# Performance work log

Hardware: AMD Instinct MI355X
Metric: run time of the kernel (lower is better)

Reference implementation:

```python
import jax, jax.numpy as jnp
import numpy as np

EPS = 1e-6
TEMP_GEO = 0.07
W_LOCAL = 0.5
W_SHARP = 0.5


def _l2norm(x):
    return x / jnp.clip(jnp.linalg.norm(x, axis=-1, keepdims=True), 1e-12)


def setup_inputs() -> dict:
    key = jax.random.key(0)
    ks = jax.random.split(key, 6)
    B, L, S, C = 8, 1024, 1024, 128
    N, P = 8, 256
    q_geo = _l2norm(jax.random.normal(ks[0], (B, L, C), jnp.float32))
    geo_pos = _l2norm(jax.random.normal(ks[1], (B, S, C), jnp.float32))
    label = jax.random.randint(ks[2], (B, L, S), 0, 2, jnp.int32)
    q_cl = jax.random.normal(ks[3], (N, P, C), jnp.float32)
    cl_pos = jax.random.normal(ks[4], (N, P, C), jnp.float32)
    idx = jax.random.randint(ks[5], (N,), 0, P, jnp.int32)
    return {"q_geo": q_geo, "q_cl": q_cl, "geo_pos": geo_pos,
            "cl_pos": cl_pos, "label": label, "idx": idx}


def _masked_mean(v, m):
    # per-sample mean over the [L,S] plane of entries where m is True
    m = m.astype(v.dtype)
    return jnp.sum(v * m, axis=(1, 2)) / jnp.maximum(jnp.sum(m, axis=(1, 2)), 1.0)


def _loftr_loss(conf, label):
    # standard LoFTR coarse CE loss (LoFTRLoss source absent from repo snippet)
    conf = jnp.clip(conf, EPS, 1.0 - EPS)
    pos = label == 1
    neg = label == 0
    pos_loss = _masked_mean(-jnp.log(conf), pos)          # [B]
    neg_loss = _masked_mean(-jnp.log(1.0 - conf), neg)    # [B]
    loss = pos_loss + neg_loss
    return jnp.mean(loss), jnp.mean(pos_loss), jnp.mean(neg_loss)


def _geometric_loss(q, k, label):
    sim = jnp.einsum('blc,bsc->bls', q, k) / TEMP_GEO        # [B,L,S]
    conf = jax.nn.softmax(sim, axis=1) * jax.nn.softmax(sim, axis=2)
    return _loftr_loss(conf, label)


def _sharpness_loss(q, k, label):
    sim = (1.0 + jnp.einsum('blc,bsc->bls', q, k)) / 2.0     # [B,L,S]
    # column stats (over L, dim=0 per sample) -> sharpness1 [B,S]
    s1 = (jnp.max(sim, axis=1) - jnp.mean(sim, axis=1)) / jnp.std(sim, axis=1, ddof=1)
    sharp1 = jax.nn.softmax(s1, axis=-1)
    # row stats (over S, dim=1 per sample) -> sharpness2 [B,L]
    s2 = (jnp.max(sim, axis=2) - jnp.mean(sim, axis=2)) / jnp.std(sim, axis=2, ddof=1)
    sharp2 = jax.nn.softmax(s2, axis=-1)
    simc = jnp.clip(sim, EPS, 1.0 - EPS)
    nll = -jnp.log(simc)
    pos = (label == 1).astype(simc.dtype)
    neg = (label == 0)
    loss1 = jnp.sum(nll * sharp1[:, None, :] * pos, axis=(1, 2))   # [B]
    loss2 = jnp.sum(nll * sharp2[:, :, None] * pos, axis=(1, 2))   # [B]
    loss3 = _masked_mean(-jnp.log(1.0 - simc), neg)                # [B]
    losses = (loss1 + loss2) / 2.0 + loss3
    return sharp1, jnp.mean(losses)


def _contrast_loss(q, all_k):
    # intended math of GeCoContrast: full cosine matrix, diag positives, tail negatives
    N = q.shape[0]
    sim = (1.0 + _l2norm(q) @ _l2norm(all_k).T) / 2.0   # [N, M]
    sim = jnp.clip(sim, EPS, 1.0 - EPS)
    l_pos = jnp.diagonal(sim[:, :N])                    # [N]
    l_neg = sim[:, N:]                                  # [N, M-N]
    return (jnp.mean(-jnp.log(l_pos)) + jnp.mean(-jnp.log(1.0 - l_neg))) / 2.0


def _forward(q_geo, q_cl, geo_pos, cl_pos, label, idx):
    loss_geo, geo_pos_loss, geo_neg_loss = _geometric_loss(q_geo, geo_pos, label)
    sharpness, loss_sharp = _sharpness_loss(q_geo, geo_pos, label)
    loss_geo = ((1.0 - W_SHARP) * loss_geo + W_SHARP * loss_sharp) * W_LOCAL

    N, P, C = q_cl.shape
    ar = jnp.arange(N)
    q_sel = q_cl[ar, idx]                               # [N,C]
    sel = cl_pos[ar, idx]                               # [N,C] positives moved to slot 0
    first = cl_pos[:, 0, :]
    swapped = cl_pos.at[ar, idx].set(first).at[:, 0, :].set(sel)
    cl_pos_save = sel
    all_k = jnp.concatenate([swapped[:, 0, :],
                             swapped[:, 1:, :].reshape(N * (P - 1), C)], axis=0)
    loss_cl = _contrast_loss(q_sel, all_k) * (1.0 - W_LOCAL)

    total = loss_geo + loss_cl
    return (sharpness, cl_pos_save, total, geo_pos_loss, geo_neg_loss, loss_sharp, loss_cl)


def reference(q_geo, q_cl, geo_pos, cl_pos, label, idx):
    return _forward(q_geo, q_cl, geo_pos, cl_pos, label, idx)
```

## Files before the change

kernel.cpp:

```cpp
#include <hip/hip_runtime.h>
#include <math.h>

#define BB 8
#define LL 1024
#define SS 1024
#define CC 128
#define NN 8
#define PP 256

static constexpr float EPS       = 1e-6f;
static constexpr float ONE_M_EPS = 1.0f - 1e-6f;
static constexpr float INV_T     = 1.0f / 0.07f;
static constexpr float NLL_MAX   = 13.815511f;
static constexpr float NLL_MIN   = 1.0000005e-6f;

static constexpr size_t DOTSZ      = (size_t)BB * LL * SS;
static constexpr size_t OFF_LSER   = DOTSZ;
static constexpr size_t OFF_LSEC   = DOTSZ + 16384;
static constexpr size_t OFF_SHARP2 = DOTSZ + 32768;
static constexpr size_t OFF_RP     = DOTSZ + 40960;
static constexpr size_t OFF_CP     = OFF_RP + 1048576;
static constexpr size_t OFF_ACC    = OFF_CP + 524288;
static constexpr size_t OFF_ACCCL  = OFF_ACC + 48;
static constexpr size_t OFF_QN     = OFF_ACC + 64;

static constexpr int OUT_CLSAVE = 8192;
static constexpr int OUT_SCAL   = 9216;

typedef __bf16 bf16x8 __attribute__((ext_vector_type(8)));
typedef float  floatx4 __attribute__((ext_vector_type(4)));

__device__ __forceinline__ void split_f4(float4 x,
                                         unsigned& hp0, unsigned& hp1,
                                         unsigned& lp0, unsigned& lp1) {
    unsigned u0 = __builtin_bit_cast(unsigned, x.x);
    unsigned u1 = __builtin_bit_cast(unsigned, x.y);
    unsigned u2 = __builtin_bit_cast(unsigned, x.z);
    unsigned u3 = __builtin_bit_cast(unsigned, x.w);
    unsigned r0 = u0 + 0x7FFFu + ((u0 >> 16) & 1u);
    unsigned r1 = u1 + 0x7FFFu + ((u1 >> 16) & 1u);
    unsigned r2 = u2 + 0x7FFFu + ((u2 >> 16) & 1u);
    unsigned r3 = u3 + 0x7FFFu + ((u3 >> 16) & 1u);
    float s0 = x.x - __builtin_bit_cast(float, r0 & 0xFFFF0000u);
    float s1 = x.y - __builtin_bit_cast(float, r1 & 0xFFFF0000u);
    float s2 = x.z - __builtin_bit_cast(float, r2 & 0xFFFF0000u);
    float s3 = x.w - __builtin_bit_cast(float, r3 & 0xFFFF0000u);
    hp0 = __builtin_amdgcn_perm(r1, r0, 0x07060302u);
    hp1 = __builtin_amdgcn_perm(r3, r2, 0x07060302u);
    lp0 = __builtin_amdgcn_perm(__builtin_bit_cast(unsigned, s1),
                                __builtin_bit_cast(unsigned, s0), 0x07060302u);
    lp1 = __builtin_amdgcn_perm(__builtin_bit_cast(unsigned, s3),
                                __builtin_bit_cast(unsigned, s2), 0x07060302u);
}

__global__ __launch_bounds__(512) void gemm_dot(const float* __restrict__ A,
                                                const float* __restrict__ Bm,
                                                const float* __restrict__ q_cl,
                                                const float* __restrict__ cl_pos,
                                                const int* __restrict__ idx,
                                                float* __restrict__ out,
                                                float* __restrict__ dot,
                                                float* __restrict__ ws) {
    __shared__ __align__(16) char lds[65536];

    int tid  = threadIdx.x;
    int lane = tid & 63;
    int w    = tid >> 6;

    if (blockIdx.x == 512) {
        if (tid < 52) ws[OFF_ACC + tid] = 0.0f;
        int n = w;
        if (n < NN) {
            int in = idx[n];
            const float* q = q_cl + ((size_t)(n * PP + in)) * CC;
            float2 qv = *(const float2*)(q + 2 * lane);
            float ss = qv.x * qv.x + qv.y * qv.y;
            for (int o = 32; o; o >>= 1) ss += __shfl_xor(ss, o);
            float inv = 1.0f / fmaxf(sqrtf(ss), 1e-12f);
            *(float2*)(ws + OFF_QN + n * 128 + 2 * lane) = make_float2(qv.x * inv, qv.y * inv);
            const float* cp = cl_pos + ((size_t)(n * PP + in)) * CC;
            float2 cv = *(const float2*)(cp + 2 * lane);
            *(float2*)(out + OUT_CLSAVE + n * 128 + 2 * lane) = cv;
        }
        return;
    }

    int t  = blockIdx.x;
    int b  = t >> 6;
    int rm = t & 63;
    int bl = rm >> 3, bs = rm & 7;
    int R0 = bl * 128, C0 = bs * 128;

    const float* Ab = A  + ((size_t)(b * 1024 + R0)) * CC;
    const float* Bb = Bm + ((size_t)(b * 1024 + C0)) * CC;

    const float* srcu[2];
    int hib[2], lob[2];
#pragma unroll
    for (int u = 0; u < 2; u++) {
        int g   = u * 512 + tid;
        int mat = g >> 9;
        int r   = (g >> 2) & 127;
        int c8  = g & 3;
        srcu[u] = (mat ? Bb : Ab) + (size_t)r * CC + c8 * 8;
        int base = mat * 16384 + r * 128;
        int sw   = r & 7;
        hib[u] = base + ((c8 ^ sw) * 16);
        lob[u] = base + (((c8 + 4) ^ sw) * 16);
    }

    int fl   = lane & 15;
    int quad = lane >> 4;
    int wr   = w >> 2, wc = w & 3;
    int Rw   = wr * 64, Cw = wc * 32;

    floatx4 acc[4][2];
#pragma unroll
    for (int i = 0; i < 4; i++)
#pragma unroll
        for (int j = 0; j < 2; j++) acc[i][j] = (floatx4){0.f, 0.f, 0.f, 0.f};

    float4 e0[2], e1[2], o0[2], o1[2];
#pragma unroll
    for (int u = 0; u < 2; u++) {
        e0[u] = *(const float4*)(srcu[u]);
        e1[u] = *(const float4*)(srcu[u] + 4);
        o0[u] = *(const float4*)(srcu[u] + 32);
        o1[u] = *(const float4*)(srcu[u] + 36);
    }
#pragma unroll
    for (int u = 0; u < 2; u++) {
        unsigned h0, h1, h2, h3, l0, l1, l2, l3;
        split_f4(e0[u], h0, h1, l0, l1); split_f4(e1[u], h2, h3, l2, l3);
        *(uint4*)(&lds[hib[u]]) = make_uint4(h0, h1, h2, h3);
        *(uint4*)(&lds[lob[u]]) = make_uint4(l0, l1, l2, l3);
        split_f4(o0[u], h0, h1, l0, l1); split_f4(o1[u], h2, h3, l2, l3);
        *(uint4*)(&lds[32768 + hib[u]]) = make_uint4(h0, h1, h2, h3);
        *(uint4*)(&lds[32768 + lob[u]]) = make_uint4(l0, l1, l2, l3);
    }
    __syncthreads();

#pragma unroll
    for (int half = 0; half < 2; half++) {
        if (half == 0) {
#pragma unroll
            for (int u = 0; u < 2; u++) {
                e0[u] = *(const float4*)(srcu[u] + 64);
                e1[u] = *(const float4*)(srcu[u] + 68);
                o0[u] = *(const float4*)(srcu[u] + 96);
                o1[u] = *(const float4*)(srcu[u] + 100);
            }
        }
#pragma unroll
        for (int kk = 0; kk < 2; kk++) {
            const char* la = lds + kk * 32768;
            const char* lb = la + 16384;
            bf16x8 ah[4], al[4];
#pragma unroll
            for (int mt = 0; mt < 4; mt++) {
                int row = Rw + mt * 16 + fl;
                int sw  = row & 7;
                ah[mt] = *(const bf16x8*)(la + row * 128 + ((quad ^ sw) * 16));
                al[mt] = *(const bf16x8*)(la + row * 128 + (((quad + 4) ^ sw) * 16));
            }
#pragma unroll
            for (int nt = 0; nt < 2; nt++) {
                int row = Cw + nt * 16 + fl;
                int sw  = row & 7;
                bf16x8 bh  = *(const bf16x8*)(lb + row * 128 + ((quad ^ sw) * 16));
                bf16x8 blo = *(const bf16x8*)(lb + row * 128 + (((quad + 4) ^ sw) * 16));
#pragma unroll
                for (int mt = 0; mt < 4; mt++) {
                    acc[mt][nt] = __builtin_amdgcn_mfma_f32_16x16x32_bf16(ah[mt], bh,  acc[mt][nt], 0, 0, 0);
                    acc[mt][nt] = __builtin_amdgcn_mfma_f32_16x16x32_bf16(ah[mt], blo, acc[mt][nt], 0, 0, 0);
                    acc[mt][nt] = __builtin_amdgcn_mfma_f32_16x16x32_bf16(al[mt], bh,  acc[mt][nt], 0, 0, 0);
                }
            }
        }
        __syncthreads();
        if (half == 0) {
#pragma unroll
            for (int u = 0; u < 2; u++) {
                unsigned h0, h1, h2, h3, l0, l1, l2, l3;
                split_f4(e0[u], h0, h1, l0, l1); split_f4(e1[u], h2, h3, l2, l3);
                *(uint4*)(&lds[hib[u]]) = make_uint4(h0, h1, h2, h3);
                *(uint4*)(&lds[lob[u]]) = make_uint4(l0, l1, l2, l3);
                split_f4(o0[u], h0, h1, l0, l1); split_f4(o1[u], h2, h3, l2, l3);
                *(uint4*)(&lds[32768 + hib[u]]) = make_uint4(h0, h1, h2, h3);
                *(uint4*)(&lds[32768 + lob[u]]) = make_uint4(l0, l1, l2, l3);
            }
            __syncthreads();
        }
    }

    float* Lf = (float*)lds;
#pragma unroll
    for (int mt = 0; mt < 4; mt++)
#pragma unroll
        for (int nt = 0; nt < 2; nt++) {
            int cl = Cw + nt * 16 + fl;
#pragma unroll
            for (int r = 0; r < 4; r++) {
                int rl = Rw + mt * 16 + quad * 4 + r;
                Lf[rl * 128 + cl] = acc[mt][nt][r];
            }
        }
    __syncthreads();
    float* drow = dot + ((size_t)(b * 1024 + R0)) * 1024 + C0;
#pragma unroll
    for (int it = 0; it < 8; it++) {
        int tg = it * 512 + tid;
        int rl = tg >> 5;
        int cf = (tg & 31) * 4;
        float4 v = *(const float4*)(Lf + rl * 128 + cf);
        *(float4*)(drow + (size_t)rl * 1024 + cf) = v;
    }

    int stile = bs * 4 + wc;
    int ltile = bl * 2 + wr;
    float ces[2], cmx[2], csm[2], csq[2];
#pragma unroll
    for (int nt = 0; nt < 2; nt++) { ces[nt] = 0.f; cmx[nt] = -1e30f; csm[nt] = 0.f; csq[nt] = 0.f; }
#pragma unroll
    for (int mt = 0; mt < 4; mt++) {
#pragma unroll
        for (int r = 0; r < 4; r++) {
            float es = 0.f, mx = -1e30f, sm = 0.f, sq = 0.f;
#pragma unroll
            for (int nt = 0; nt < 2; nt++) {
                float d  = acc[mt][nt][r];
                float e  = __expf(d * INV_T);
                float s2 = fmaf(0.5f, d, 0.5f);
                es += e; mx = fmaxf(mx, s2); sm += s2; sq += s2 * s2;
                ces[nt] += e; cmx[nt] = fmaxf(cmx[nt], s2); csm[nt] += s2; csq[nt] += s2 * s2;
            }
            for (int o = 1; o < 16; o <<= 1) {
                es += __shfl_xor(es, o);
                mx = fmaxf(mx, __shfl_xor(mx, o));
                sm += __shfl_xor(sm, o);
                sq += __shfl_xor(sq, o);
            }
            if (fl == 0) {
                int row = R0 + Rw + mt * 16 + quad * 4 + r;
                *(float4*)(ws + OFF_RP + (((size_t)(b * 32 + stile)) * 1024 + row) * 4) =
                    make_float4(es, mx, sm, sq);
            }
        }
    }
#pragma unroll
    for (int nt = 0; nt < 2; nt++) {
        float es = ces[nt], mx = cmx[nt], sm = csm[nt], sq = csq[nt];
        for (int o = 16; o < 64; o <<= 1) {
            es += __shfl_xor(es, o);
            mx = fmaxf(mx, __shfl_xor(mx, o));
            sm += __shfl_xor(sm, o);
            sq += __shfl_xor(sq, o);
        }
        if (quad == 0) {
            int col = C0 + Cw + nt * 16 + fl;
            *(float4*)(ws + OFF_CP + (((size_t)(b * 16 + ltile)) * 1024 + col) * 4) =
                make_float4(es, mx, sm, sq);
        }
    }
}

__global__ __launch_bounds__(256) void mid(const float* __restrict__ cl_pos,
                                           const int* __restrict__ idx,
                                           float* __restrict__ ws,
                                           float* __restrict__ out) {
    int q   = blockIdx.x;
    int tid = threadIdx.x;
    int lane = tid & 63, wid = tid >> 6;

    if (q < 16) {
        bool docol = (q < 8);
        int b = q & 7;
        const float* pb = ws + (docol ? (OFF_CP + (size_t)b * 16 * 1024 * 4)
                                      : (OFF_RP + (size_t)b * 32 * 1024 * 4));
        float* lse = ws + (docol ? OFF_LSEC : OFF_LSER) + (size_t)b * 1024;
        float zs[4];
        float mxall = -1e30f;
#pragma unroll
        for (int r = 0; r < 4; r++) {
            int i = tid + r * 256;
            const float* base = pb + (size_t)i * 4;
            float es = 0.f, mx = -1e30f, sm = 0.f, sq = 0.f;
#pragma unroll
            for (int t = 0; t < 16; t++) {
                float4 v = *(const float4*)(base + (size_t)t * 4096);
                es += v.x; mx = fmaxf(mx, v.y); sm += v.z; sq += v.w;
            }
            if (!docol) {
#pragma unroll
                for (int t = 16; t < 32; t++) {
                    float4 v = *(const float4*)(base + (size_t)t * 4096);
                    es += v.x; mx = fmaxf(mx, v.y); sm += v.z; sq += v.w;
                }
            }
            float mean = sm * (1.0f / 1024.0f);
            float var  = (sq - sm * sm * (1.0f / 1024.0f)) * (1.0f / 1023.0f);
            zs[r] = (mx - mean) / sqrtf(fmaxf(var, 1e-30f));
            mxall = fmaxf(mxall, zs[r]);
            lse[i] = __logf(es);
        }
        __shared__ float sb[4];
        __shared__ float red;
        float mx = mxall;
        for (int o = 32; o; o >>= 1) mx = fmaxf(mx, __shfl_xor(mx, o));
        if (!lane) sb[wid] = mx;
        __syncthreads();
        if (tid == 0) red = fmaxf(fmaxf(sb[0], sb[1]), fmaxf(sb[2], sb[3]));
        __syncthreads();
        mx = red;
        float e[4]; float smv = 0.f;
#pragma unroll
        for (int r = 0; r < 4; r++) { e[r] = __expf(zs[r] - mx); smv += e[r]; }
        for (int o = 32; o; o >>= 1) smv += __shfl_xor(smv, o);
        __syncthreads();
        if (!lane) sb[wid] = smv;
        __syncthreads();
        if (tid == 0) red = sb[0] + sb[1] + sb[2] + sb[3];
        __syncthreads();
        float inv = 1.0f / red;
        float* dst = docol ? (out + (size_t)b * 1024) : (ws + OFF_SHARP2 + (size_t)b * 1024);
#pragma unroll
        for (int r = 0; r < 4; r++) dst[tid + r * 256] = e[r] * inv;
    } else {
        int j = (q - 16) * 4 + wid;
        int m, p;
        if (j < NN) {
            m = j; p = idx[j];
        } else {
            int jj = j - NN;
            m = jj / (PP - 1);
            p = 1 + (jj - m * (PP - 1));
            if (p == idx[m]) p = 0;
        }
        const float* k = cl_pos + ((size_t)(m * PP + p)) * CC;
        float2 kv = *(const float2*)(k + 2 * lane);
        float ksq = kv.x * kv.x + kv.y * kv.y;
        for (int o = 32; o; o >>= 1) ksq += __shfl_xor(ksq, o);
        float invkn = 1.0f / fmaxf(sqrtf(ksq), 1e-12f);
        float pos = 0.0f, neg = 0.0f;
        if (j < NN) {
            const float2 qv = *(const float2*)(ws + OFF_QN + j * 128 + 2 * lane);
            float dt = qv.x * kv.x + qv.y * kv.y;
            for (int o = 32; o; o >>= 1) dt += __shfl_xor(dt, o);
            float sim = fminf(fmaxf(fmaf(0.5f * invkn, dt, 0.5f), EPS), ONE_M_EPS);
            pos = -__logf(sim);
        } else {
#pragma unroll
            for (int n = 0; n < NN; n++) {
                const float2 qv = *(const float2*)(ws + OFF_QN + n * 128 + 2 * lane);
                float dt = qv.x * kv.x + qv.y * kv.y;
                for (int o = 32; o; o >>= 1) dt += __shfl_xor(dt, o);
                float om = fminf(fmaxf(fmaf(-0.5f * invkn, dt, 0.5f), EPS), ONE_M_EPS);
                neg -= __logf(om);
            }
        }
        __shared__ float cb[2][4];
        if (!lane) { cb[0][wid] = pos; cb[1][wid] = neg; }
        __syncthreads();
        if (tid == 0) {
            float ps = cb[0][0] + cb[0][1] + cb[0][2] + cb[0][3];
            float ng = cb[1][0] + cb[1][1] + cb[1][2] + cb[1][3];
            if (ps != 0.0f) atomicAdd(ws + OFF_ACCCL + 0, ps);
            if (ng != 0.0f) atomicAdd(ws + OFF_ACCCL + 1, ng);
        }
    }
}

__device__ __forceinline__ void proc_elem(float d, int lab, float lcj, float sh1j,
                                          float lr, float s2v,
                                          float& posg, float& negg, float& l1, float& l2,
                                          float& negs, float& pcf) {
    float t = lr + lcj - d * (2.0f * INV_T);
    bool  pos   = (lab == 1);
    float isPos = pos ? 1.0f : 0.0f;
    float isNeg = 1.0f - isPos;
    float tp   = fminf(fmaxf(t, NLL_MIN), NLL_MAX);
    float simc = fminf(fmaxf(fmaf(0.5f, d, 0.5f), EPS), ONE_M_EPS);
    float om   = fminf(fmaxf(fmaf(-0.5f, d, 0.5f), EPS), ONE_M_EPS);
    float x    = pos ? simc : om;
    float nllx = -__logf(x);
    float cf   = fminf(fmaxf(__expf(-t), EPS), ONE_M_EPS);
    float wi   = pos ? 1.0f : (1.0f - cf);
    float nllw = -__logf(wi);
    posg += isPos * tp;
    l1   += isPos * nllx * sh1j;
    l2   += isPos * nllx * s2v;
    pcf  += isPos;
    negg += isNeg * nllw;
    negs += isNeg * nllx;
}

__global__ __launch_bounds__(256) void main_loss(const float* __restrict__ dot,
                                                 const int* __restrict__ label,
                                                 const float* __restrict__ sharp1,
                                                 float* __restrict__ ws) {
    int b = blockIdx.y;
    int l0 = blockIdx.x * 4;
    int s = threadIdx.x * 4;
    float4 lc4 = *(const float4*)(ws + OFF_LSEC + (size_t)b * 1024 + s);
    float4 sh1 = *(const float4*)(sharp1 + (size_t)b * 1024 + s);
    float4 lr4 = *(const float4*)(ws + OFF_LSER + (size_t)b * 1024 + l0);
    float4 s24 = *(const float4*)(ws + OFF_SHARP2 + (size_t)b * 1024 + l0);
    size_t base0 = ((size_t)(b * 1024 + l0)) * 1024 + s;
    float4 d4[4]; int4 lb[4];
#pragma unroll
    for (int r = 0; r < 4; r++) {
        d4[r] = *(const float4*)(dot + base0 + (size_t)r * 1024);
        lb[r] = *(const int4*)(label + base0 + (size_t)r * 1024);
    }
    float lrv[4] = {lr4.x, lr4.y, lr4.z, lr4.w};
    float s2v[4] = {s24.x, s24.y, s24.z, s24.w};
    float posg = 0, negg = 0, l1 = 0, l2 = 0, negs = 0, pcf = 0;
#pragma unroll
    for (int r = 0; r < 4; r++) {
        proc_elem(d4[r].x, lb[r].x, lc4.x, sh1.x, lrv[r], s2v[r], posg, negg, l1, l2, negs, pcf);
        proc_elem(d4[r].y, lb[r].y, lc4.y, sh1.y, lrv[r], s2v[r], posg, negg, l1, l2, negs, pcf);
        proc_elem(d4[r].z, lb[r].z, lc4.z, sh1.z, lrv[r], s2v[r], posg, negg, l1, l2, negs, pcf);
        proc_elem(d4[r].w, lb[r].w, lc4.w, sh1.w, lrv[r], s2v[r], posg, negg, l1, l2, negs, pcf);
    }
    float vals[6] = {posg, negg, l1, l2, negs, pcf};
    __shared__ float sb[6][4];
    int lane = threadIdx.x & 63, wid = threadIdx.x >> 6;
#pragma unroll
    for (int k = 0; k < 6; k++) {
        float v = vals[k];
        for (int o = 32; o; o >>= 1) v += __shfl_xor(v, o);
        if (!lane) sb[k][wid] = v;
    }
    __syncthreads();
    if (threadIdx.x < 6) {
        float r = sb[threadIdx.x][0] + sb[threadIdx.x][1] + sb[threadIdx.x][2] + sb[threadIdx.x][3];
        atomicAdd(ws + OFF_ACC + (size_t)b * 6 + threadIdx.x, r);
    }
}

__global__ void finalize(float* __restrict__ out, const float* __restrict__ ws) {
    if (threadIdx.x != 0) return;
    float gp = 0, gn = 0, lsh = 0;
    for (int b = 0; b < 8; b++) {
        const float* a = ws + OFF_ACC + (size_t)b * 6;
        float pc = a[5];
        float nc = (float)((size_t)LL * SS) - pc;
        gp += a[0] / fmaxf(pc, 1.0f);
        gn += a[1] / fmaxf(nc, 1.0f);
        lsh += (a[2] + a[3]) * 0.5f + a[4] / fmaxf(nc, 1.0f);
    }
    gp *= 0.125f; gn *= 0.125f; lsh *= 0.125f;
    float lgeo = gp + gn;
    float lgw = (0.5f * lgeo + 0.5f * lsh) * 0.5f;
    float clp = ws[OFF_ACCCL + 0] / 8.0f;
    float cln = ws[OFF_ACCCL + 1] / (8.0f * 2040.0f);
    float lcl = (clp + cln) * 0.5f * 0.5f;
    out[OUT_SCAL + 0] = lgw + lcl;
    out[OUT_SCAL + 1] = gp;
    out[OUT_SCAL + 2] = gn;
    out[OUT_SCAL + 3] = lsh;
    out[OUT_SCAL + 4] = lcl;
}

extern "C" void kernel_launch(void* const* d_in, const int* in_sizes, int n_in,
                              void* d_out, int out_size, void* d_ws, size_t ws_size,
                              hipStream_t stream) {
    const float* q_geo   = (const float*)d_in[0];
    const float* q_cl    = (const float*)d_in[1];
    const float* geo_pos = (const float*)d_in[2];
    const float* cl_pos  = (const float*)d_in[3];
    const int*   label   = (const int*)d_in[4];
    const int*   idx     = (const int*)d_in[5];
    float* out = (float*)d_out;
    float* ws  = (float*)d_ws;
    float* dot = ws;

    gemm_dot<<<dim3(513), dim3(512), 0, stream>>>(q_geo, geo_pos, q_cl, cl_pos, idx, out, dot, ws);
    mid<<<dim3(528), dim3(256), 0, stream>>>(cl_pos, idx, ws, out);
    main_loss<<<dim3(256, 8), dim3(256), 0, stream>>>(dot, label, out, ws);
    finalize<<<dim3(1), dim3(64), 0, stream>>>(out, ws);
}
```

Before: 152.4 us.

## Fuse all stages into one persistent kernel with grid barriers, keep dot tile in LDS

```diff
diff --git a/kernel.cpp b/kernel.cpp
--- a/kernel.cpp
+++ b/kernel.cpp
@@ -14,15 +14,19 @@
 static constexpr float NLL_MAX   = 13.815511f;
 static constexpr float NLL_MIN   = 1.0000005e-6f;
 
-static constexpr size_t DOTSZ      = (size_t)BB * LL * SS;
-static constexpr size_t OFF_LSER   = DOTSZ;
-static constexpr size_t OFF_LSEC   = DOTSZ + 16384;
-static constexpr size_t OFF_SHARP2 = DOTSZ + 32768;
-static constexpr size_t OFF_RP     = DOTSZ + 40960;
+static constexpr size_t OFF_LSER   = 0;
+static constexpr size_t OFF_LSEC   = 8192;
+static constexpr size_t OFF_SHARP2 = 16384;
+static constexpr size_t OFF_RP     = 24576;
 static constexpr size_t OFF_CP     = OFF_RP + 1048576;
 static constexpr size_t OFF_ACC    = OFF_CP + 524288;
 static constexpr size_t OFF_ACCCL  = OFF_ACC + 48;
-static constexpr size_t OFF_QN     = OFF_ACC + 64;
+static constexpr size_t OFF_SYNC   = OFF_ACC + 64;
+static constexpr size_t OFF_QN     = OFF_ACC + 128;
+static constexpr size_t OFF_R2     = OFF_QN + 1024;
+static constexpr size_t OFF_R3     = OFF_R2 + 512;
+
+static constexpr unsigned MAGIC = 0x1337C0DEu;
 
 static constexpr int OUT_CLSAVE = 8192;
 static constexpr int OUT_SCAL   = 9216;
@@ -53,321 +57,16 @@
                                 __builtin_bit_cast(unsigned, s2), 0x07060302u);
 }
 
-__global__ __launch_bounds__(512) void gemm_dot(const float* __restrict__ A,
-                                                const float* __restrict__ Bm,
-                                                const float* __restrict__ q_cl,
-                                                const float* __restrict__ cl_pos,
-                                                const int* __restrict__ idx,
-                                                float* __restrict__ out,
-                                                float* __restrict__ dot,
-                                                float* __restrict__ ws) {
-    __shared__ __align__(16) char lds[65536];
-
-    int tid  = threadIdx.x;
-    int lane = tid & 63;
-    int w    = tid >> 6;
-
-    if (blockIdx.x == 512) {
-        if (tid < 52) ws[OFF_ACC + tid] = 0.0f;
-        int n = w;
-        if (n < NN) {
-            int in = idx[n];
-            const float* q = q_cl + ((size_t)(n * PP + in)) * CC;
-            float2 qv = *(const float2*)(q + 2 * lane);
-            float ss = qv.x * qv.x + qv.y * qv.y;
-            for (int o = 32; o; o >>= 1) ss += __shfl_xor(ss, o);
-            float inv = 1.0f / fmaxf(sqrtf(ss), 1e-12f);
-            *(float2*)(ws + OFF_QN + n * 128 + 2 * lane) = make_float2(qv.x * inv, qv.y * inv);
-            const float* cp = cl_pos + ((size_t)(n * PP + in)) * CC;
-            float2 cv = *(const float2*)(cp + 2 * lane);
-            *(float2*)(out + OUT_CLSAVE + n * 128 + 2 * lane) = cv;
-        }
-        return;
-    }
-
-    int t  = blockIdx.x;
-    int b  = t >> 6;
-    int rm = t & 63;
-    int bl = rm >> 3, bs = rm & 7;
-    int R0 = bl * 128, C0 = bs * 128;
-
-    const float* Ab = A  + ((size_t)(b * 1024 + R0)) * CC;
-    const float* Bb = Bm + ((size_t)(b * 1024 + C0)) * CC;
-
-    const float* srcu[2];
-    int hib[2], lob[2];
-#pragma unroll
-    for (int u = 0; u < 2; u++) {
-        int g   = u * 512 + tid;
-        int mat = g >> 9;
-        int r   = (g >> 2) & 127;
-        int c8  = g & 3;
-        srcu[u] = (mat ? Bb : Ab) + (size_t)r * CC + c8 * 8;
-        int base = mat * 16384 + r * 128;
-        int sw   = r & 7;
-        hib[u] = base + ((c8 ^ sw) * 16);
-        lob[u] = base + (((c8 + 4) ^ sw) * 16);
-    }
-
-    int fl   = lane & 15;
-    int quad = lane >> 4;
-    int wr   = w >> 2, wc = w & 3;
-    int Rw   = wr * 64, Cw = wc * 32;
-
-    floatx4 acc[4][2];
-#pragma unroll
-    for (int i = 0; i < 4; i++)
-#pragma unroll
-        for (int j = 0; j < 2; j++) acc[i][j] = (floatx4){0.f, 0.f, 0.f, 0.f};
-
-    float4 e0[2], e1[2], o0[2], o1[2];
-#pragma unroll
-    for (int u = 0; u < 2; u++) {
-        e0[u] = *(const float4*)(srcu[u]);
-        e1[u] = *(const float4*)(srcu[u] + 4);
-        o0[u] = *(const float4*)(srcu[u] + 32);
-        o1[u] = *(const float4*)(srcu[u] + 36);
-    }
-#pragma unroll
-    for (int u = 0; u < 2; u++) {
-        unsigned h0, h1, h2, h3, l0, l1, l2, l3;
-        split_f4(e0[u], h0, h1, l0, l1); split_f4(e1[u], h2, h3, l2, l3);
-        *(uint4*)(&lds[hib[u]]) = make_uint4(h0, h1, h2, h3);
-        *(uint4*)(&lds[lob[u]]) = make_uint4(l0, l1, l2, l3);
-        split_f4(o0[u], h0, h1, l0, l1); split_f4(o1[u], h2, h3, l2, l3);
-        *(uint4*)(&lds[32768 + hib[u]]) = make_uint4(h0, h1, h2, h3);
-        *(uint4*)(&lds[32768 + lob[u]]) = make_uint4(l0, l1, l2, l3);
-    }
+__device__ __forceinline__ void gsync(unsigned* sc, int id) {
     __syncthreads();
-
-#pragma unroll
-    for (int half = 0; half < 2; half++) {
-        if (half == 0) {
-#pragma unroll
-            for (int u = 0; u < 2; u++) {
-                e0[u] = *(const float4*)(srcu[u] + 64);
-                e1[u] = *(const float4*)(srcu[u] + 68);
-                o0[u] = *(const float4*)(srcu[u] + 96);
-                o1[u] = *(const float4*)(srcu[u] + 100);
-            }
-        }
-#pragma unroll
-        for (int kk = 0; kk < 2; kk++) {
-            const char* la = lds + kk * 32768;
-            const char* lb = la + 16384;
-            bf16x8 ah[4], al[4];
-#pragma unroll
-            for (int mt = 0; mt < 4; mt++) {
-                int row = Rw + mt * 16 + fl;
-                int sw  = row & 7;
-                ah[mt] = *(const bf16x8*)(la + row * 128 + ((quad ^ sw) * 16));
-                al[mt] = *(const bf16x8*)(la + row * 128 + (((quad + 4) ^ sw) * 16));
-            }
-#pragma unroll
-            for (int nt = 0; nt < 2; nt++) {
-                int row = Cw + nt * 16 + fl;
-                int sw  = row & 7;
-                bf16x8 bh  = *(const bf16x8*)(lb + row * 128 + ((quad ^ sw) * 16));
-                bf16x8 blo = *(const bf16x8*)(lb + row * 128 + (((quad + 4) ^ sw) * 16));
-#pragma unroll
-                for (int mt = 0; mt < 4; mt++) {
-                    acc[mt][nt] = __builtin_amdgcn_mfma_f32_16x16x32_bf16(ah[mt], bh,  acc[mt][nt], 0, 0, 0);
-                    acc[mt][nt] = __builtin_amdgcn_mfma_f32_16x16x32_bf16(ah[mt], blo, acc[mt][nt], 0, 0, 0);
-                    acc[mt][nt] = __builtin_amdgcn_mfma_f32_16x16x32_bf16(al[mt], bh,  acc[mt][nt], 0, 0, 0);
-                }
-            }
-        }
-        __syncthreads();
-        if (half == 0) {
-#pragma unroll
-            for (int u = 0; u < 2; u++) {
-                unsigned h0, h1, h2, h3, l0, l1, l2, l3;
-                split_f4(e0[u], h0, h1, l0, l1); split_f4(e1[u], h2, h3, l2, l3);
-                *(uint4*)(&lds[hib[u]]) = make_uint4(h0, h1, h2, h3);
-                *(uint4*)(&lds[lob[u]]) = make_uint4(l0, l1, l2, l3);
-                split_f4(o0[u], h0, h1, l0, l1); split_f4(o1[u], h2, h3, l2, l3);
-                *(uint4*)(&lds[32768 + hib[u]]) = make_uint4(h0, h1, h2, h3);
-                *(uint4*)(&lds[32768 + lob[u]]) = make_uint4(l0, l1, l2, l3);
-            }
-            __syncthreads();
-        }
-    }
-
-    float* Lf = (float*)lds;
-#pragma unroll
-    for (int mt = 0; mt < 4; mt++)
-#pragma unroll
-        for (int nt = 0; nt < 2; nt++) {
-            int cl = Cw + nt * 16 + fl;
-#pragma unroll
-            for (int r = 0; r < 4; r++) {
-                int rl = Rw + mt * 16 + quad * 4 + r;
-                Lf[rl * 128 + cl] = acc[mt][nt][r];
-            }
-        }
+    if (threadIdx.x == 0) {
+        unsigned* c = sc + id;
+        __hip_atomic_fetch_add(c, 1u, __ATOMIC_ACQ_REL, __HIP_MEMORY_SCOPE_AGENT);
+        while (__hip_atomic_load(c, __ATOMIC_RELAXED, __HIP_MEMORY_SCOPE_AGENT) < 512u)
+            __builtin_amdgcn_s_sleep(8);
+        (void)__hip_atomic_load(c, __ATOMIC_ACQUIRE, __HIP_MEMORY_SCOPE_AGENT);
+    }
     __syncthreads();
-    float* drow = dot + ((size_t)(b * 1024 + R0)) * 1024 + C0;
-#pragma unroll
-    for (int it = 0; it < 8; it++) {
-        int tg = it * 512 + tid;
-        int rl = tg >> 5;
-        int cf = (tg & 31) * 4;
-        float4 v = *(const float4*)(Lf + rl * 128 + cf);
-        *(float4*)(drow + (size_t)rl * 1024 + cf) = v;
-    }
-
-    int stile = bs * 4 + wc;
-    int ltile = bl * 2 + wr;
-    float ces[2], cmx[2], csm[2], csq[2];
-#pragma unroll
-    for (int nt = 0; nt < 2; nt++) { ces[nt] = 0.f; cmx[nt] = -1e30f; csm[nt] = 0.f; csq[nt] = 0.f; }
-#pragma unroll
-    for (int mt = 0; mt < 4; mt++) {
-#pragma unroll
-        for (int r = 0; r < 4; r++) {
-            float es = 0.f, mx = -1e30f, sm = 0.f, sq = 0.f;
-#pragma unroll
-            for (int nt = 0; nt < 2; nt++) {
-                float d  = acc[mt][nt][r];
-                float e  = __expf(d * INV_T);
-                float s2 = fmaf(0.5f, d, 0.5f);
-                es += e; mx = fmaxf(mx, s2); sm += s2; sq += s2 * s2;
-                ces[nt] += e; cmx[nt] = fmaxf(cmx[nt], s2); csm[nt] += s2; csq[nt] += s2 * s2;
-            }
-            for (int o = 1; o < 16; o <<= 1) {
-                es += __shfl_xor(es, o);
-                mx = fmaxf(mx, __shfl_xor(mx, o));
-                sm += __shfl_xor(sm, o);
-                sq += __shfl_xor(sq, o);
-            }
-            if (fl == 0) {
-                int row = R0 + Rw + mt * 16 + quad * 4 + r;
-                *(float4*)(ws + OFF_RP + (((size_t)(b * 32 + stile)) * 1024 + row) * 4) =
-                    make_float4(es, mx, sm, sq);
-            }
-        }
-    }
-#pragma unroll
-    for (int nt = 0; nt < 2; nt++) {
-        float es = ces[nt], mx = cmx[nt], sm = csm[nt], sq = csq[nt];
-        for (int o = 16; o < 64; o <<= 1) {
-            es += __shfl_xor(es, o);
-            mx = fmaxf(mx, __shfl_xor(mx, o));
-            sm += __shfl_xor(sm, o);
-            sq += __shfl_xor(sq, o);
-        }
-        if (quad == 0) {
-            int col = C0 + Cw + nt * 16 + fl;
-            *(float4*)(ws + OFF_CP + (((size_t)(b * 16 + ltile)) * 1024 + col) * 4) =
-                make_float4(es, mx, sm, sq);
-        }
-    }
-}
-
-__global__ __launch_bounds__(256) void mid(const float* __restrict__ cl_pos,
-                                           const int* __restrict__ idx,
-                                           float* __restrict__ ws,
-                                           float* __restrict__ out) {
-    int q   = blockIdx.x;
-    int tid = threadIdx.x;
-    int lane = tid & 63, wid = tid >> 6;
-
-    if (q < 16) {
-        bool docol = (q < 8);
-        int b = q & 7;
-        const float* pb = ws + (docol ? (OFF_CP + (size_t)b * 16 * 1024 * 4)
-                                      : (OFF_RP + (size_t)b * 32 * 1024 * 4));
-        float* lse = ws + (docol ? OFF_LSEC : OFF_LSER) + (size_t)b * 1024;
-        float zs[4];
-        float mxall = -1e30f;
-#pragma unroll
-        for (int r = 0; r < 4; r++) {
-            int i = tid + r * 256;
-            const float* base = pb + (size_t)i * 4;
-            float es = 0.f, mx = -1e30f, sm = 0.f, sq = 0.f;
-#pragma unroll
-            for (int t = 0; t < 16; t++) {
-                float4 v = *(const float4*)(base + (size_t)t * 4096);
-                es += v.x; mx = fmaxf(mx, v.y); sm += v.z; sq += v.w;
-            }
-            if (!docol) {
-#pragma unroll
-                for (int t = 16; t < 32; t++) {
-                    float4 v = *(const float4*)(base + (size_t)t * 4096);
-                    es += v.x; mx = fmaxf(mx, v.y); sm += v.z; sq += v.w;
-                }
-            }
-            float mean = sm * (1.0f / 1024.0f);
-            float var  = (sq - sm * sm * (1.0f / 1024.0f)) * (1.0f / 1023.0f);
-            zs[r] = (mx - mean) / sqrtf(fmaxf(var, 1e-30f));
-            mxall = fmaxf(mxall, zs[r]);
-            lse[i] = __logf(es);
-        }
-        __shared__ float sb[4];
-        __shared__ float red;
-        float mx = mxall;
-        for (int o = 32; o; o >>= 1) mx = fmaxf(mx, __shfl_xor(mx, o));
-        if (!lane) sb[wid] = mx;
-        __syncthreads();
-        if (tid == 0) red = fmaxf(fmaxf(sb[0], sb[1]), fmaxf(sb[2], sb[3]));
-        __syncthreads();
-        mx = red;
-        float e[4]; float smv = 0.f;
-#pragma unroll
-        for (int r = 0; r < 4; r++) { e[r] = __expf(zs[r] - mx); smv += e[r]; }
-        for (int o = 32; o; o >>= 1) smv += __shfl_xor(smv, o);
-        __syncthreads();
-        if (!lane) sb[wid] = smv;
-        __syncthreads();
-        if (tid == 0) red = sb[0] + sb[1] + sb[2] + sb[3];
-        __syncthreads();
-        float inv = 1.0f / red;
-        float* dst = docol ? (out + (size_t)b * 1024) : (ws + OFF_SHARP2 + (size_t)b * 1024);
-#pragma unroll
-        for (int r = 0; r < 4; r++) dst[tid + r * 256] = e[r] * inv;
-    } else {
-        int j = (q - 16) * 4 + wid;
-        int m, p;
-        if (j < NN) {
-            m = j; p = idx[j];
-        } else {
-            int jj = j - NN;
-            m = jj / (PP - 1);
-            p = 1 + (jj - m * (PP - 1));
-            if (p == idx[m]) p = 0;
-        }
-        const float* k = cl_pos + ((size_t)(m * PP + p)) * CC;
-        float2 kv = *(const float2*)(k + 2 * lane);
-        float ksq = kv.x * kv.x + kv.y * kv.y;
-        for (int o = 32; o; o >>= 1) ksq += __shfl_xor(ksq, o);
-        float invkn = 1.0f / fmaxf(sqrtf(ksq), 1e-12f);
-        float pos = 0.0f, neg = 0.0f;
-        if (j < NN) {
-            const float2 qv = *(const float2*)(ws + OFF_QN + j * 128 + 2 * lane);
-            float dt = qv.x * kv.x + qv.y * kv.y;
-            for (int o = 32; o; o >>= 1) dt += __shfl_xor(dt, o);
-            float sim = fminf(fmaxf(fmaf(0.5f * invkn, dt, 0.5f), EPS), ONE_M_EPS);
-            pos = -__logf(sim);
-        } else {
-#pragma unroll
-            for (int n = 0; n < NN; n++) {
-                const float2 qv = *(const float2*)(ws + OFF_QN + n * 128 + 2 * lane);
-                float dt = qv.x * kv.x + qv.y * kv.y;
-                for (int o = 32; o; o >>= 1) dt += __shfl_xor(dt, o);
-                float om = fminf(fmaxf(fmaf(-0.5f * invkn, dt, 0.5f), EPS), ONE_M_EPS);
-                neg -= __logf(om);
-            }
-        }
-        __shared__ float cb[2][4];
-        if (!lane) { cb[0][wid] = pos; cb[1][wid] = neg; }
-        __syncthreads();
-        if (tid == 0) {
-            float ps = cb[0][0] + cb[0][1] + cb[0][2] + cb[0][3];
-            float ng = cb[1][0] + cb[1][1] + cb[1][2] + cb[1][3];
-            if (ps != 0.0f) atomicAdd(ws + OFF_ACCCL + 0, ps);
-            if (ng != 0.0f) atomicAdd(ws + OFF_ACCCL + 1, ng);
-        }
-    }
 }
 
 __device__ __forceinline__ void proc_elem(float d, int lab, float lcj, float sh1j,
@@ -394,72 +93,416 @@
     negs += isNeg * nllx;
 }
 
-__global__ __launch_bounds__(256) void main_loss(const float* __restrict__ dot,
-                                                 const int* __restrict__ label,
-                                                 const float* __restrict__ sharp1,
-                                                 float* __restrict__ ws) {
-    int b = blockIdx.y;
-    int l0 = blockIdx.x * 4;
-    int s = threadIdx.x * 4;
-    float4 lc4 = *(const float4*)(ws + OFF_LSEC + (size_t)b * 1024 + s);
-    float4 sh1 = *(const float4*)(sharp1 + (size_t)b * 1024 + s);
-    float4 lr4 = *(const float4*)(ws + OFF_LSER + (size_t)b * 1024 + l0);
-    float4 s24 = *(const float4*)(ws + OFF_SHARP2 + (size_t)b * 1024 + l0);
-    size_t base0 = ((size_t)(b * 1024 + l0)) * 1024 + s;
-    float4 d4[4]; int4 lb[4];
-#pragma unroll
-    for (int r = 0; r < 4; r++) {
-        d4[r] = *(const float4*)(dot + base0 + (size_t)r * 1024);
-        lb[r] = *(const int4*)(label + base0 + (size_t)r * 1024);
-    }
-    float lrv[4] = {lr4.x, lr4.y, lr4.z, lr4.w};
-    float s2v[4] = {s24.x, s24.y, s24.z, s24.w};
-    float posg = 0, negg = 0, l1 = 0, l2 = 0, negs = 0, pcf = 0;
-#pragma unroll
-    for (int r = 0; r < 4; r++) {
-        proc_elem(d4[r].x, lb[r].x, lc4.x, sh1.x, lrv[r], s2v[r], posg, negg, l1, l2, negs, pcf);
-        proc_elem(d4[r].y, lb[r].y, lc4.y, sh1.y, lrv[r], s2v[r], posg, negg, l1, l2, negs, pcf);
-        proc_elem(d4[r].z, lb[r].z, lc4.z, sh1.z, lrv[r], s2v[r], posg, negg, l1, l2, negs, pcf);
-        proc_elem(d4[r].w, lb[r].w, lc4.w, sh1.w, lrv[r], s2v[r], posg, negg, l1, l2, negs, pcf);
-    }
-    float vals[6] = {posg, negg, l1, l2, negs, pcf};
-    __shared__ float sb[6][4];
-    int lane = threadIdx.x & 63, wid = threadIdx.x >> 6;
-#pragma unroll
-    for (int k = 0; k < 6; k++) {
-        float v = vals[k];
-        for (int o = 32; o; o >>= 1) v += __shfl_xor(v, o);
-        if (!lane) sb[k][wid] = v;
+__global__ __launch_bounds__(512, 4) void mega(const float* __restrict__ A,
+                                               const float* __restrict__ Bm,
+                                               const float* __restrict__ q_cl,
+                                               const float* __restrict__ cl_pos,
+                                               const int* __restrict__ label,
+                                               const int* __restrict__ idx,
+                                               float* __restrict__ out,
+                                               float* __restrict__ ws) {
+    __shared__ __align__(16) char lds[65536];
+
+    int tid  = threadIdx.x;
+    int lane = tid & 63;
+    int w    = tid >> 6;
+    int t    = blockIdx.x;
+    unsigned* sc = (unsigned*)(ws + OFF_SYNC);
+
+    if (t == 0) {
+        if (tid == 0) {
+            __hip_atomic_store(sc + 1, 0u, __ATOMIC_RELAXED, __HIP_MEMORY_SCOPE_AGENT);
+            __hip_atomic_store(sc + 2, 0u, __ATOMIC_RELAXED, __HIP_MEMORY_SCOPE_AGENT);
+            __hip_atomic_store(sc + 3, 0u, __ATOMIC_RELAXED, __HIP_MEMORY_SCOPE_AGENT);
+            __hip_atomic_store(sc + 0, MAGIC, __ATOMIC_RELEASE, __HIP_MEMORY_SCOPE_AGENT);
+        }
+        if (tid < 50)
+            __hip_atomic_store(ws + OFF_ACC + tid, 0.0f, __ATOMIC_RELAXED, __HIP_MEMORY_SCOPE_AGENT);
+        {
+            int n = w;
+            int in = idx[n];
+            const float* q = q_cl + ((size_t)(n * PP + in)) * CC;
+            float2 qv = *(const float2*)(q + 2 * lane);
+            float ss = qv.x * qv.x + qv.y * qv.y;
+            for (int o = 32; o; o >>= 1) ss += __shfl_xor(ss, o);
+            float inv = 1.0f / fmaxf(sqrtf(ss), 1e-12f);
+            *(float2*)(ws + OFF_QN + n * 128 + 2 * lane) = make_float2(qv.x * inv, qv.y * inv);
+            const float* cp = cl_pos + ((size_t)(n * PP + in)) * CC;
+            float2 cv = *(const float2*)(cp + 2 * lane);
+            *(float2*)(out + OUT_CLSAVE + n * 128 + 2 * lane) = cv;
+        }
+    } else if (tid == 0) {
+        while (__hip_atomic_load(sc, __ATOMIC_RELAXED, __HIP_MEMORY_SCOPE_AGENT) != MAGIC)
+            __builtin_amdgcn_s_sleep(8);
+        (void)__hip_atomic_load(sc, __ATOMIC_ACQUIRE, __HIP_MEMORY_SCOPE_AGENT);
     }
     __syncthreads();
-    if (threadIdx.x < 6) {
-        float r = sb[threadIdx.x][0] + sb[threadIdx.x][1] + sb[threadIdx.x][2] + sb[threadIdx.x][3];
-        atomicAdd(ws + OFF_ACC + (size_t)b * 6 + threadIdx.x, r);
-    }
-}
-
-__global__ void finalize(float* __restrict__ out, const float* __restrict__ ws) {
-    if (threadIdx.x != 0) return;
-    float gp = 0, gn = 0, lsh = 0;
-    for (int b = 0; b < 8; b++) {
-        const float* a = ws + OFF_ACC + (size_t)b * 6;
-        float pc = a[5];
-        float nc = (float)((size_t)LL * SS) - pc;
-        gp += a[0] / fmaxf(pc, 1.0f);
-        gn += a[1] / fmaxf(nc, 1.0f);
-        lsh += (a[2] + a[3]) * 0.5f + a[4] / fmaxf(nc, 1.0f);
-    }
-    gp *= 0.125f; gn *= 0.125f; lsh *= 0.125f;
-    float lgeo = gp + gn;
-    float lgw = (0.5f * lgeo + 0.5f * lsh) * 0.5f;
-    float clp = ws[OFF_ACCCL + 0] / 8.0f;
-    float cln = ws[OFF_ACCCL + 1] / (8.0f * 2040.0f);
-    float lcl = (clp + cln) * 0.5f * 0.5f;
-    out[OUT_SCAL + 0] = lgw + lcl;
-    out[OUT_SCAL + 1] = gp;
-    out[OUT_SCAL + 2] = gn;
-    out[OUT_SCAL + 3] = lsh;
-    out[OUT_SCAL + 4] = lcl;
+
+    int b  = t >> 6;
+    int rm = t & 63;
+    int bl = rm >> 3, bs = rm & 7;
+    int R0 = bl * 128, C0 = bs * 128;
+
+    const float* Ab = A  + ((size_t)(b * 1024 + R0)) * CC;
+    const float* Bb = Bm + ((size_t)(b * 1024 + C0)) * CC;
+
+    const float* srcu[2];
+    int hib[2], lob[2];
+#pragma unroll
+    for (int u = 0; u < 2; u++) {
+        int g   = u * 512 + tid;
+        int mat = g >> 9;
+        int r   = (g >> 2) & 127;
+        int c8  = g & 3;
+        srcu[u] = (mat ? Bb : Ab) + (size_t)r * CC + c8 * 8;
+        int base = mat * 16384 + r * 128;
+        int sw   = r & 7;
+        hib[u] = base + ((c8 ^ sw) * 16);
+        lob[u] = base + (((c8 + 4) ^ sw) * 16);
+    }
+
+    int fl   = lane & 15;
+    int quad = lane >> 4;
+    int wr   = w >> 2, wc = w & 3;
+    int Rw   = wr * 64, Cw = wc * 32;
+
+    {
+        floatx4 acc[4][2];
+#pragma unroll
+        for (int i = 0; i < 4; i++)
+#pragma unroll
+            for (int j = 0; j < 2; j++) acc[i][j] = (floatx4){0.f, 0.f, 0.f, 0.f};
+
+        float4 e0[2], e1[2], o0[2], o1[2];
+#pragma unroll
+        for (int u = 0; u < 2; u++) {
+            e0[u] = *(const float4*)(srcu[u]);
+            e1[u] = *(const float4*)(srcu[u] + 4);
+            o0[u] = *(const float4*)(srcu[u] + 32);
+            o1[u] = *(const float4*)(srcu[u] + 36);
+        }
+#pragma unroll
+        for (int u = 0; u < 2; u++) {
+            unsigned h0, h1, h2, h3, l0, l1, l2, l3;
+            split_f4(e0[u], h0, h1, l0, l1); split_f4(e1[u], h2, h3, l2, l3);
+            *(uint4*)(&lds[hib[u]]) = make_uint4(h0, h1, h2, h3);
+            *(uint4*)(&lds[lob[u]]) = make_uint4(l0, l1, l2, l3);
+            split_f4(o0[u], h0, h1, l0, l1); split_f4(o1[u], h2, h3, l2, l3);
+            *(uint4*)(&lds[32768 + hib[u]]) = make_uint4(h0, h1, h2, h3);
+            *(uint4*)(&lds[32768 + lob[u]]) = make_uint4(l0, l1, l2, l3);
+        }
+        __syncthreads();
+
+#pragma unroll
+        for (int half = 0; half < 2; half++) {
+            if (half == 0) {
+#pragma unroll
+                for (int u = 0; u < 2; u++) {
+                    e0[u] = *(const float4*)(srcu[u] + 64);
+                    e1[u] = *(const float4*)(srcu[u] + 68);
+                    o0[u] = *(const float4*)(srcu[u] + 96);
+                    o1[u] = *(const float4*)(srcu[u] + 100);
+                }
+            }
+#pragma unroll
+            for (int kk = 0; kk < 2; kk++) {
+                const char* la = lds + kk * 32768;
+                const char* lb = la + 16384;
+                bf16x8 ah[4], al[4];
+#pragma unroll
+                for (int mt = 0; mt < 4; mt++) {
+                    int row = Rw + mt * 16 + fl;
+                    int sw  = row & 7;
+                    ah[mt] = *(const bf16x8*)(la + row * 128 + ((quad ^ sw) * 16));
+                    al[mt] = *(const bf16x8*)(la + row * 128 + (((quad + 4) ^ sw) * 16));
+                }
+#pragma unroll
+                for (int nt = 0; nt < 2; nt++) {
+                    int row = Cw + nt * 16 + fl;
+                    int sw  = row & 7;
+                    bf16x8 bh  = *(const bf16x8*)(lb + row * 128 + ((quad ^ sw) * 16));
+                    bf16x8 blo = *(const bf16x8*)(lb + row * 128 + (((quad + 4) ^ sw) * 16));
+#pragma unroll
+                    for (int mt = 0; mt < 4; mt++) {
+                        acc[mt][nt] = __builtin_amdgcn_mfma_f32_16x16x32_bf16(ah[mt], bh,  acc[mt][nt], 0, 0, 0);
+                        acc[mt][nt] = __builtin_amdgcn_mfma_f32_16x16x32_bf16(ah[mt], blo, acc[mt][nt], 0, 0, 0);
+                        acc[mt][nt] = __builtin_amdgcn_mfma_f32_16x16x32_bf16(al[mt], bh,  acc[mt][nt], 0, 0, 0);
+                    }
+                }
+            }
+            __syncthreads();
+            if (half == 0) {
+#pragma unroll
+                for (int u = 0; u < 2; u++) {
+                    unsigned h0, h1, h2, h3, l0, l1, l2, l3;
+                    split_f4(e0[u], h0, h1, l0, l1); split_f4(e1[u], h2, h3, l2, l3);
+                    *(uint4*)(&lds[hib[u]]) = make_uint4(h0, h1, h2, h3);
+                    *(uint4*)(&lds[lob[u]]) = make_uint4(l0, l1, l2, l3);
+                    split_f4(o0[u], h0, h1, l0, l1); split_f4(o1[u], h2, h3, l2, l3);
+                    *(uint4*)(&lds[32768 + hib[u]]) = make_uint4(h0, h1, h2, h3);
+                    *(uint4*)(&lds[32768 + lob[u]]) = make_uint4(l0, l1, l2, l3);
+                }
+                __syncthreads();
+            }
+        }
+
+        float* Lf = (float*)lds;
+#pragma unroll
+        for (int mt = 0; mt < 4; mt++)
+#pragma unroll
+            for (int nt = 0; nt < 2; nt++) {
+                int cl = Cw + nt * 16 + fl;
+#pragma unroll
+                for (int r = 0; r < 4; r++)
+                    Lf[(Rw + mt * 16 + quad * 4 + r) * 128 + cl] = acc[mt][nt][r];
+            }
+
+        int stile = bs * 4 + wc;
+        int ltile = bl * 2 + wr;
+        float ces[2], cmx[2], csm[2], csq[2];
+#pragma unroll
+        for (int nt = 0; nt < 2; nt++) { ces[nt] = 0.f; cmx[nt] = -1e30f; csm[nt] = 0.f; csq[nt] = 0.f; }
+#pragma unroll
+        for (int mt = 0; mt < 4; mt++) {
+#pragma unroll
+            for (int r = 0; r < 4; r++) {
+                float es = 0.f, mx = -1e30f, sm = 0.f, sq = 0.f;
+#pragma unroll
+                for (int nt = 0; nt < 2; nt++) {
+                    float d  = acc[mt][nt][r];
+                    float e  = __expf(d * INV_T);
+                    float s2 = fmaf(0.5f, d, 0.5f);
+                    es += e; mx = fmaxf(mx, s2); sm += s2; sq += s2 * s2;
+                    ces[nt] += e; cmx[nt] = fmaxf(cmx[nt], s2); csm[nt] += s2; csq[nt] += s2 * s2;
+                }
+                for (int o = 1; o < 16; o <<= 1) {
+                    es += __shfl_xor(es, o);
+                    mx = fmaxf(mx, __shfl_xor(mx, o));
+                    sm += __shfl_xor(sm, o);
+                    sq += __shfl_xor(sq, o);
+                }
+                if (fl == 0) {
+                    int row = R0 + Rw + mt * 16 + quad * 4 + r;
+                    *(float4*)(ws + OFF_RP + (((size_t)(b * 32 + stile)) * 1024 + row) * 4) =
+                        make_float4(es, mx, sm, sq);
+                }
+            }
+        }
+#pragma unroll
+        for (int nt = 0; nt < 2; nt++) {
+            float es = ces[nt], mx = cmx[nt], sm = csm[nt], sq = csq[nt];
+            for (int o = 16; o < 64; o <<= 1) {
+                es += __shfl_xor(es, o);
+                mx = fmaxf(mx, __shfl_xor(mx, o));
+                sm += __shfl_xor(sm, o);
+                sq += __shfl_xor(sq, o);
+            }
+            if (quad == 0) {
+                int col = C0 + Cw + nt * 16 + fl;
+                *(float4*)(ws + OFF_CP + (((size_t)(b * 16 + ltile)) * 1024 + col) * 4) =
+                    make_float4(es, mx, sm, sq);
+            }
+        }
+    }
+
+    gsync(sc, 1);
+
+    if (t < 16) {
+        bool docol = (t < 8);
+        int bq = t & 7;
+        const float* pb = ws + (docol ? (OFF_CP + (size_t)bq * 16 * 1024 * 4)
+                                      : (OFF_RP + (size_t)bq * 32 * 1024 * 4));
+        float* lse = ws + (docol ? OFF_LSEC : OFF_LSER) + (size_t)bq * 1024;
+        float* red = ws + OFF_R2 + (size_t)t * 18;
+        float zs[2];
+        float mxall = -1e30f;
+#pragma unroll
+        for (int r = 0; r < 2; r++) {
+            int i = tid + r * 512;
+            const float* base = pb + (size_t)i * 4;
+            float es = 0.f, mx = -1e30f, sm = 0.f, sq = 0.f;
+#pragma unroll
+            for (int tt = 0; tt < 16; tt++) {
+                float4 v = *(const float4*)(base + (size_t)tt * 4096);
+                es += v.x; mx = fmaxf(mx, v.y); sm += v.z; sq += v.w;
+            }
+            if (!docol) {
+#pragma unroll
+                for (int tt = 16; tt < 32; tt++) {
+                    float4 v = *(const float4*)(base + (size_t)tt * 4096);
+                    es += v.x; mx = fmaxf(mx, v.y); sm += v.z; sq += v.w;
+                }
+            }
+            float mean = sm * (1.0f / 1024.0f);
+            float var  = (sq - sm * sm * (1.0f / 1024.0f)) * (1.0f / 1023.0f);
+            zs[r] = (mx - mean) / sqrtf(fmaxf(var, 1e-30f));
+            mxall = fmaxf(mxall, zs[r]);
+            lse[i] = __logf(es);
+        }
+        float mx = mxall;
+        for (int o = 32; o; o >>= 1) mx = fmaxf(mx, __shfl_xor(mx, o));
+        if (!lane) red[w] = mx;
+        __syncthreads();
+        if (tid == 0) {
+            float m = red[0];
+            for (int k = 1; k < 8; k++) m = fmaxf(m, red[k]);
+            red[16] = m;
+        }
+        __syncthreads();
+        mx = red[16];
+        float e[2]; float smv = 0.f;
+#pragma unroll
+        for (int r = 0; r < 2; r++) { e[r] = __expf(zs[r] - mx); smv += e[r]; }
+        for (int o = 32; o; o >>= 1) smv += __shfl_xor(smv, o);
+        if (!lane) red[8 + w] = smv;
+        __syncthreads();
+        if (tid == 0) {
+            float s = red[8];
+            for (int k = 1; k < 8; k++) s += red[8 + k];
+            red[17] = s;
+        }
+        __syncthreads();
+        float inv = 1.0f / red[17];
+        float* dst = docol ? (out + (size_t)bq * 1024) : (ws + OFF_SHARP2 + (size_t)bq * 1024);
+#pragma unroll
+        for (int r = 0; r < 2; r++) dst[tid + r * 512] = e[r] * inv;
+    } else if (t < 81) {
+        int j = (t - 16) * 8 + w;
+        int m, p;
+        if (j < NN) {
+            m = j; p = idx[j];
+        } else {
+            int jj = j - NN;
+            m = jj / (PP - 1);
+            p = 1 + (jj - m * (PP - 1));
+            if (p == idx[m]) p = 0;
+        }
+        const float* k = cl_pos + ((size_t)(m * PP + p)) * CC;
+        float2 kv = *(const float2*)(k + 2 * lane);
+        float ksq = kv.x * kv.x + kv.y * kv.y;
+        for (int o = 32; o; o >>= 1) ksq += __shfl_xor(ksq, o);
+        float invkn = 1.0f / fmaxf(sqrtf(ksq), 1e-12f);
+        if (j < NN) {
+            const float2 qv = *(const float2*)(ws + OFF_QN + j * 128 + 2 * lane);
+            float dt = qv.x * kv.x + qv.y * kv.y;
+            for (int o = 32; o; o >>= 1) dt += __shfl_xor(dt, o);
+            float sim = fminf(fmaxf(fmaf(0.5f * invkn, dt, 0.5f), EPS), ONE_M_EPS);
+            if (lane == 0) atomicAdd(ws + OFF_ACCCL + 0, -__logf(sim));
+        } else {
+            float neg = 0.0f;
+#pragma unroll
+            for (int n = 0; n < NN; n++) {
+                const float2 qv = *(const float2*)(ws + OFF_QN + n * 128 + 2 * lane);
+                float dt = qv.x * kv.x + qv.y * kv.y;
+                for (int o = 32; o; o >>= 1) dt += __shfl_xor(dt, o);
+                float om = fminf(fmaxf(fmaf(-0.5f * invkn, dt, 0.5f), EPS), ONE_M_EPS);
+                neg -= __logf(om);
+            }
+            if (lane == 0) atomicAdd(ws + OFF_ACCCL + 1, neg);
+        }
+    }
+
+    gsync(sc, 2);
+
+    {
+        float* Lf = (float*)lds;
+        floatx4 acc[4][2];
+#pragma unroll
+        for (int mt = 0; mt < 4; mt++)
+#pragma unroll
+            for (int nt = 0; nt < 2; nt++) {
+                int cl = Cw + nt * 16 + fl;
+#pragma unroll
+                for (int r = 0; r < 4; r++)
+                    acc[mt][nt][r] = Lf[(Rw + mt * 16 + quad * 4 + r) * 128 + cl];
+            }
+        __syncthreads();
+
+        int* Li = (int*)lds;
+        const int* lrow = label + ((size_t)(b * 1024 + R0)) * 1024 + C0;
+#pragma unroll
+        for (int it = 0; it < 8; it++) {
+            int g  = it * 512 + tid;
+            int rr = g >> 5;
+            int cc = (g & 31) * 4;
+            *(int4*)(Li + rr * 128 + cc) = *(const int4*)(lrow + (size_t)rr * 1024 + cc);
+        }
+        __syncthreads();
+
+        floatx4 lr4[4], s24[4];
+#pragma unroll
+        for (int mt = 0; mt < 4; mt++) {
+            int row = R0 + Rw + mt * 16 + quad * 4;
+            lr4[mt] = *(const floatx4*)(ws + OFF_LSER + (size_t)b * 1024 + row);
+            s24[mt] = *(const floatx4*)(ws + OFF_SHARP2 + (size_t)b * 1024 + row);
+        }
+        float lcv[2], sh1v[2];
+#pragma unroll
+        for (int nt = 0; nt < 2; nt++) {
+            int col = C0 + Cw + nt * 16 + fl;
+            lcv[nt]  = ws[OFF_LSEC + (size_t)b * 1024 + col];
+            sh1v[nt] = out[(size_t)b * 1024 + col];
+        }
+
+        float posg = 0, negg = 0, l1 = 0, l2 = 0, negs = 0, pcf = 0;
+#pragma unroll
+        for (int mt = 0; mt < 4; mt++)
+#pragma unroll
+            for (int r = 0; r < 4; r++) {
+                int rl = (Rw + mt * 16 + quad * 4 + r) * 128;
+#pragma unroll
+                for (int nt = 0; nt < 2; nt++) {
+                    int lab = Li[rl + Cw + nt * 16 + fl];
+                    proc_elem(acc[mt][nt][r], lab, lcv[nt], sh1v[nt], lr4[mt][r], s24[mt][r],
+                              posg, negg, l1, l2, negs, pcf);
+                }
+            }
+
+        float vals[6] = {posg, negg, l1, l2, negs, pcf};
+        float* red3 = ws + OFF_R3 + (size_t)t * 48;
+#pragma unroll
+        for (int k = 0; k < 6; k++) {
+            float v = vals[k];
+            for (int o = 32; o; o >>= 1) v += __shfl_xor(v, o);
+            if (!lane) red3[k * 8 + w] = v;
+        }
+        __syncthreads();
+        if (tid < 6) {
+            float r = 0.f;
+#pragma unroll
+            for (int k = 0; k < 8; k++) r += red3[tid * 8 + k];
+            atomicAdd(ws + OFF_ACC + (size_t)b * 6 + tid, r);
+        }
+    }
+
+    gsync(sc, 3);
+
+    if (t == 0 && tid == 0) {
+        float gp = 0, gn = 0, lsh = 0;
+        for (int b2 = 0; b2 < 8; b2++) {
+            float a0 = __hip_atomic_load(ws + OFF_ACC + b2 * 6 + 0, __ATOMIC_RELAXED, __HIP_MEMORY_SCOPE_AGENT);
+            float a1 = __hip_atomic_load(ws + OFF_ACC + b2 * 6 + 1, __ATOMIC_RELAXED, __HIP_MEMORY_SCOPE_AGENT);
+            float a2 = __hip_atomic_load(ws + OFF_ACC + b2 * 6 + 2, __ATOMIC_RELAXED, __HIP_MEMORY_SCOPE_AGENT);
+            float a3 = __hip_atomic_load(ws + OFF_ACC + b2 * 6 + 3, __ATOMIC_RELAXED, __HIP_MEMORY_SCOPE_AGENT);
+            float a4 = __hip_atomic_load(ws + OFF_ACC + b2 * 6 + 4, __ATOMIC_RELAXED, __HIP_MEMORY_SCOPE_AGENT);
+            float pc = __hip_atomic_load(ws + OFF_ACC + b2 * 6 + 5, __ATOMIC_RELAXED, __HIP_MEMORY_SCOPE_AGENT);
+            float nc = (float)((size_t)LL * SS) - pc;
+            gp += a0 / fmaxf(pc, 1.0f);
+            gn += a1 / fmaxf(nc, 1.0f);
+            lsh += (a2 + a3) * 0.5f + a4 / fmaxf(nc, 1.0f);
+        }
+        gp *= 0.125f; gn *= 0.125f; lsh *= 0.125f;
+        float lgeo = gp + gn;
+        float lgw = (0.5f * lgeo + 0.5f * lsh) * 0.5f;
+        float clp = __hip_atomic_load(ws + OFF_ACCCL + 0, __ATOMIC_RELAXED, __HIP_MEMORY_SCOPE_AGENT) / 8.0f;
+        float cln = __hip_atomic_load(ws + OFF_ACCCL + 1, __ATOMIC_RELAXED, __HIP_MEMORY_SCOPE_AGENT) / (8.0f * 2040.0f);
+        float lcl = (clp + cln) * 0.5f * 0.5f;
+        out[OUT_SCAL + 0] = lgw + lcl;
+        out[OUT_SCAL + 1] = gp;
+        out[OUT_SCAL + 2] = gn;
+        out[OUT_SCAL + 3] = lsh;
+        out[OUT_SCAL + 4] = lcl;
+    }
 }
 
 extern "C" void kernel_launch(void* const* d_in, const int* in_sizes, int n_in,
@@ -473,10 +516,6 @@
     const int*   idx     = (const int*)d_in[5];
     float* out = (float*)d_out;
     float* ws  = (float*)d_ws;
-    float* dot = ws;
-
-    gemm_dot<<<dim3(513), dim3(512), 0, stream>>>(q_geo, geo_pos, q_cl, cl_pos, idx, out, dot, ws);
-    mid<<<dim3(528), dim3(256), 0, stream>>>(cl_pos, idx, ws, out);
-    main_loss<<<dim3(256, 8), dim3(256), 0, stream>>>(dot, label, out, ws);
-    finalize<<<dim3(1), dim3(64), 0, stream>>>(out, ws);
+
+    mega<<<dim3(512), dim3(512), 0, stream>>>(q_geo, geo_pos, q_cl, cl_pos, label, idx, out, ws);
 }
```

Result: slower. 244.6 us (+60.4%).
